# Kernel optimization log

Measured on AMD Instinct MI355X. Metric: run time of the kernel, lower is better.

## Reference

```python
import jax, jax.numpy as jnp
import numpy as np

BINS = 30
MMT = 0.75
LOSS_WEIGHT = 1.0
N = 16_777_216


def setup_inputs() -> dict:
    key = jax.random.key(0)
    k1, k2 = jax.random.split(key)
    pred = jax.random.normal(k1, (N,), dtype=jnp.float32)
    target = jax.random.randint(k2, (N,), 0, 2, dtype=jnp.int32)
    acc_sum = jnp.zeros((BINS,), dtype=jnp.float32)  # momentum state, zeros at first call
    return {"pred": pred, "acc_sum": acc_sum, "target": target}


def reference(pred, acc_sum, target):
    # prob = sigmoid(pred); expand to binary channels [N,2]
    prob = jax.nn.sigmoid(pred)
    t = target.astype(jnp.float32)
    x = jnp.stack([prob, 1.0 - prob], axis=1)  # [N,2]  (original reassigns pred := probs)
    y = jnp.stack([t, 1.0 - t], axis=1)        # [N,2]

    g = jnp.abs(x - y)                          # gradient-norm proxy, in [0,1]
    total = jnp.maximum(jnp.asarray(x.size, jnp.float32), 1.0)  # all label_weights == 1

    # bin assignment: loop 'g>=e[i] & g<=e[i+1]' with later-bin overwrite == floor(g*bins)
    # edges[-1] += 1e-6 means g==1 lands in last bin -> clip to BINS-1
    bin_idx = jnp.clip((g * BINS).astype(jnp.int32), 0, BINS - 1)  # [N,2]

    counts = jnp.zeros((BINS,), jnp.float32).at[bin_idx.ravel()].add(1.0)
    nonempty = counts > 0
    n = jnp.maximum(jnp.sum(nonempty.astype(jnp.float32)), 1.0)

    # momentum update of acc_sum only for populated bins
    new_acc = jnp.where(nonempty, MMT * acc_sum + (1.0 - MMT) * counts, acc_sum)
    w_bin = jnp.where(nonempty, total / jnp.maximum(new_acc, 1e-12), 0.0) / n  # [BINS]
    weights = w_bin[bin_idx]  # [N,2] scatter of per-bin weights

    # BCE-with-logits applied to x (the probabilities), matching the original
    bce = jnp.logaddexp(0.0, x) - x * y
    loss = jnp.sum(weights * bce) / total
    return loss * LOSS_WEIGHT
```

## Files before the change

kernel.cpp:

```cpp
#include <hip/hip_runtime.h>
#include <math.h>

#define BINS 30
#define FGRID 256
#define FBLOCK 1024
#define FITERS 16
#define FNCOPIES 256
#define GGRID 2048
#define GBLOCK 256
#define GNCOPIES 64
#define CPW 16
#define CSTRIDE 31
#define GSCALE 4096.0f
#define CNT_SHIFT 21
#define CNT_ONE (2u << CNT_SHIFT)
#define GMASK 0x1FFFFFu


__device__ __forceinline__ void ghmc_elem(float p, int t, unsigned int* s_hist,
                                          unsigned int copy_base)
{
    float q = __int_as_float(__float_as_int(p) ^ (t << 31));
    float e = __expf(-q);
    float g = __builtin_amdgcn_rcpf(1.0f + e);
    int b = min((int)(g * 30.0f), BINS - 1);
    unsigned int pkt = CNT_ONE | (unsigned int)(g * GSCALE);
    atomicAdd(&s_hist[copy_base + b], pkt);
}

__device__ __forceinline__ void ghmc_vec4(float4 p, int4 t, unsigned int* s_hist,
                                          unsigned int copy_base)
{
    ghmc_elem(p.x, t.x, s_hist, copy_base);
    ghmc_elem(p.y, t.y, s_hist, copy_base);
    ghmc_elem(p.z, t.z, s_hist, copy_base);
    ghmc_elem(p.w, t.w, s_hist, copy_base);
}

__global__ __launch_bounds__(FBLOCK) void ghmc_pass1_big(
    const float* __restrict__ pred, const int* __restrict__ target,
    unsigned int* __restrict__ cnt_part, float* __restrict__ gs_part)
{
    __shared__ unsigned int s_hist[FNCOPIES * CSTRIDE];
    const int tid = threadIdx.x;
    const unsigned int copy_base = (((tid >> 6) << 4) + (tid & (CPW - 1))) * CSTRIDE;

    for (int i = tid; i < FNCOPIES * CSTRIDE; i += FBLOCK) s_hist[i] = 0u;
    __syncthreads();

    const float4* p4 = reinterpret_cast<const float4*>(pred);
    const int4*   t4 = reinterpret_cast<const int4*>(target);
    const int stride = FGRID * FBLOCK;
    const int idx = blockIdx.x * FBLOCK + tid;

    float4 pA = p4[idx], pB;
    int4   tA = t4[idx], tB;
    #pragma unroll
    for (int k = 0; k < FITERS; k += 2) {
        if (k + 1 < FITERS) { pB = p4[idx + (k + 1) * stride];
                              tB = t4[idx + (k + 1) * stride]; }
        __builtin_amdgcn_sched_barrier(0);
        ghmc_vec4(pA, tA, s_hist, copy_base);
        if (k + 2 < FITERS) { pA = p4[idx + (k + 2) * stride];
                              tA = t4[idx + (k + 2) * stride]; }
        __builtin_amdgcn_sched_barrier(0);
        if (k + 1 < FITERS) ghmc_vec4(pB, tB, s_hist, copy_base);
    }

    __syncthreads();
    if (tid < BINS) {
        unsigned int cnt = 0;
        float gs = 0.0f;
        #pragma unroll 8
        for (int c = 0; c < FNCOPIES; ++c) {
            unsigned int v = s_hist[c * CSTRIDE + tid];
            cnt += v >> CNT_SHIFT;
            gs  += (float)(v & GMASK);
        }
        cnt_part[blockIdx.x * BINS + tid] = cnt;
        gs_part [blockIdx.x * BINS + tid] = gs * (1.0f / GSCALE);
    }
}

__global__ __launch_bounds__(1024) void ghmc_final_part(
    const unsigned int* __restrict__ cnt_part, const float* __restrict__ gs_part,
    const float* __restrict__ acc_sum, float* __restrict__ out, float total, int nwg)
{
    __shared__ unsigned int s_cnt[32];
    __shared__ float        s_gs[32];
    const int tid = threadIdx.x;
    const int bin = tid >> 5;
    const int j   = tid & 31;

    unsigned int c = 0;
    float        g = 0.0f;
    if (bin < BINS) {
        for (int w = j; w < nwg; w += 32) {
            c += cnt_part[w * BINS + bin];
            g += gs_part [w * BINS + bin];
        }
    }
    #pragma unroll
    for (int off = 16; off > 0; off >>= 1) {
        c += __shfl_xor(c, off);
        g += __shfl_xor(g, off);
    }
    if (bin < BINS && j == 0) { s_cnt[bin] = c; s_gs[bin] = g; }
    __syncthreads();

    if (tid < 64) {
        bool nonempty = (tid < BINS) && (s_cnt[tid] > 0u);
        float nb = fmaxf((float)__popcll(__ballot(nonempty)), 1.0f);

        float val = 0.0f;
        if (nonempty) {
            float cc    = (float)s_cnt[tid];
            float elems = 0.5f * cc;
            float gmean = s_gs[tid] / elems;
            float F = log1pf(expf(gmean)) + log1pf(expf(1.0f - gmean)) - 1.0f + gmean;
            float new_acc = 0.75f * acc_sum[tid] + 0.25f * cc;
            float w = (total / fmaxf(new_acc, 1e-12f)) / nb;
            val = w * elems * F;
        }
        #pragma unroll
        for (int off = 32; off > 0; off >>= 1) val += __shfl_down(val, off);
        if (tid == 0) out[0] = val / total;
    }
}

__global__ __launch_bounds__(GBLOCK) void ghmc_pass1_gen(
    const float* __restrict__ pred, const int* __restrict__ target,
    unsigned int* __restrict__ g_cnt, float* __restrict__ g_gsum,
    int n4, int n)
{
    __shared__ unsigned int s_hist[GNCOPIES * CSTRIDE];
    const int tid = threadIdx.x;
    const unsigned int copy_base = (((tid >> 6) << 4) + (tid & (CPW - 1))) * CSTRIDE;
    for (int i = tid; i < GNCOPIES * CSTRIDE; i += GBLOCK) s_hist[i] = 0u;
    __syncthreads();

    const int gid    = blockIdx.x * GBLOCK + tid;
    const int stride = gridDim.x * GBLOCK;
    for (int i = gid; i < n4; i += stride) {
        float4 p = reinterpret_cast<const float4*>(pred)[i];
        int4   t = reinterpret_cast<const int4*>(target)[i];
        ghmc_vec4(p, t, s_hist, copy_base);
    }
    if (blockIdx.x == 0) {
        for (int i = n4 * 4 + tid; i < n; i += GBLOCK)
            ghmc_elem(pred[i], target[i], s_hist, copy_base);
    }

    __syncthreads();
    if (tid < BINS) {
        unsigned int cnt = 0;
        float gs = 0.0f;
        #pragma unroll
        for (int c = 0; c < GNCOPIES; ++c) {
            unsigned int v = s_hist[c * CSTRIDE + tid];
            cnt += v >> CNT_SHIFT;
            gs  += (float)(v & GMASK);
        }
        atomicAdd(&g_cnt[tid], cnt);
        atomicAdd(&g_gsum[tid], gs * (1.0f / GSCALE));
    }
}

__global__ __launch_bounds__(64) void ghmc_final_atomic(
    const unsigned int* __restrict__ counts, const float* __restrict__ gsums,
    const float* __restrict__ acc_sum, float* __restrict__ out, float total)
{
    const int tid = threadIdx.x;
    bool nonempty = (tid < BINS) && (counts[tid] > 0u);
    float nb = fmaxf((float)__popcll(__ballot(nonempty)), 1.0f);

    float val = 0.0f;
    if (nonempty) {
        float cc    = (float)counts[tid];
        float elems = 0.5f * cc;
        float gmean = gsums[tid] / elems;
        float F = log1pf(expf(gmean)) + log1pf(expf(1.0f - gmean)) - 1.0f + gmean;
        float new_acc = 0.75f * acc_sum[tid] + 0.25f * cc;
        float w = (total / fmaxf(new_acc, 1e-12f)) / nb;
        val = w * elems * F;
    }
    #pragma unroll
    for (int off = 32; off > 0; off >>= 1) val += __shfl_down(val, off);
    if (tid == 0) out[0] = val / total;
}

extern "C" void kernel_launch(void* const* d_in, const int* in_sizes, int n_in,
                              void* d_out, int out_size, void* d_ws, size_t ws_size,
                              hipStream_t stream) {
    const float* pred    = (const float*)d_in[0];
    const float* acc_sum = (const float*)d_in[1];
    const int*   target  = (const int*)d_in[2];
    float* out = (float*)d_out;

    int n = in_sizes[0];
    float total = fmaxf(2.0f * (float)n, 1.0f);

    const size_t fast_ws = (size_t)FGRID * BINS * 8;
    if (n == FGRID * FBLOCK * FITERS * 4 && ws_size >= fast_ws) {
        unsigned int* cnt_part = (unsigned int*)d_ws;
        float*        gs_part  = (float*)((unsigned int*)d_ws + FGRID * BINS);
        ghmc_pass1_big<<<FGRID, FBLOCK, 0, stream>>>(pred, target, cnt_part, gs_part);
        ghmc_final_part<<<1, 1024, 0, stream>>>(cnt_part, gs_part, acc_sum, out, total, FGRID);
    } else {
        int n4 = n / 4;
        unsigned int* g_cnt  = (unsigned int*)d_ws;
        float*        g_gsum = (float*)d_ws + BINS;
        hipMemsetAsync(d_ws, 0, 2 * BINS * sizeof(float), stream);
        ghmc_pass1_gen<<<GGRID, GBLOCK, 0, stream>>>(pred, target, g_cnt, g_gsum, n4, n);
        ghmc_final_atomic<<<1, 64, 0, stream>>>(g_cnt, g_gsum, acc_sum, out, total);
    }
}
```

Measured before the change: 34.86 us.

## Deepen load pipeline with inline-asm loads and parallelize per-block histogram reduction

The main loop now issues raw global_load_dwordx4 instructions three iterations ahead into a 4-deep register ring, with explicit s_waitcnt vmcnt counts, replacing the previous two-stage software pipeline. The goal is more outstanding memory requests per thread, so HBM latency is better hidden in this bandwidth-bound pass. The end-of-block reduction over 256 histogram copies moves from 30 serial threads to 30 warps of 32 lanes, each summing 8 copies and then doing a shuffle reduction, with the grad sum kept as an integer. Hand-written asm with manual waitcnt is fragile: the compiler does not track these loads, and any vmcnt miscount can read registers before the data arrives.

```diff
diff --git a/kernel.cpp b/kernel.cpp
--- a/kernel.cpp
+++ b/kernel.cpp
@@ -6,6 +6,7 @@
 #define FBLOCK 1024
 #define FITERS 16
 #define FNCOPIES 256
+#define VSTEP (FGRID * FBLOCK * 16)
 #define GGRID 2048
 #define GBLOCK 256
 #define GNCOPIES 64
@@ -48,37 +49,55 @@
     for (int i = tid; i < FNCOPIES * CSTRIDE; i += FBLOCK) s_hist[i] = 0u;
     __syncthreads();
 
-    const float4* p4 = reinterpret_cast<const float4*>(pred);
-    const int4*   t4 = reinterpret_cast<const int4*>(target);
-    const int stride = FGRID * FBLOCK;
-    const int idx = blockIdx.x * FBLOCK + tid;
-
-    float4 pA = p4[idx], pB;
-    int4   tA = t4[idx], tB;
+    const unsigned int voff0 = (unsigned int)((blockIdx.x * FBLOCK + tid) * 16);
+
+    float4 pb[4];
+    int4   tb[4];
+
+#define ISSUE(k)                                                               \
+    do {                                                                       \
+        asm volatile("global_load_dwordx4 %0, %1, %2"                          \
+                     : "=v"(pb[(k) & 3])                                       \
+                     : "v"(voff0 + (unsigned)(k) * (unsigned)VSTEP), "s"(pred)); \
+        asm volatile("global_load_dwordx4 %0, %1, %2"                          \
+                     : "=v"(tb[(k) & 3])                                       \
+                     : "v"(voff0 + (unsigned)(k) * (unsigned)VSTEP), "s"(target)); \
+    } while (0)
+
+    ISSUE(0); ISSUE(1); ISSUE(2);
+
     #pragma unroll
-    for (int k = 0; k < FITERS; k += 2) {
-        if (k + 1 < FITERS) { pB = p4[idx + (k + 1) * stride];
-                              tB = t4[idx + (k + 1) * stride]; }
+    for (int k = 0; k < FITERS; ++k) {
+        if (k + 3 < FITERS) ISSUE(k + 3);
+        asm volatile("s_waitcnt vmcnt(%0)"
+                     :: "i"((k + 3 < FITERS) ? 6 : 2 * (FITERS - 1 - k)));
         __builtin_amdgcn_sched_barrier(0);
-        ghmc_vec4(pA, tA, s_hist, copy_base);
-        if (k + 2 < FITERS) { pA = p4[idx + (k + 2) * stride];
-                              tA = t4[idx + (k + 2) * stride]; }
-        __builtin_amdgcn_sched_barrier(0);
-        if (k + 1 < FITERS) ghmc_vec4(pB, tB, s_hist, copy_base);
-    }
-
-    __syncthreads();
-    if (tid < BINS) {
-        unsigned int cnt = 0;
-        float gs = 0.0f;
-        #pragma unroll 8
-        for (int c = 0; c < FNCOPIES; ++c) {
-            unsigned int v = s_hist[c * CSTRIDE + tid];
-            cnt += v >> CNT_SHIFT;
-            gs  += (float)(v & GMASK);
-        }
-        cnt_part[blockIdx.x * BINS + tid] = cnt;
-        gs_part [blockIdx.x * BINS + tid] = gs * (1.0f / GSCALE);
+        ghmc_vec4(pb[k & 3], tb[k & 3], s_hist, copy_base);
+    }
+#undef ISSUE
+
+    __syncthreads();
+    {
+        const int bin   = tid >> 5;
+        const int chunk = tid & 31;
+        if (bin < BINS) {
+            unsigned int c = 0, g = 0;
+            #pragma unroll
+            for (int j = 0; j < 8; ++j) {
+                unsigned int v = s_hist[(chunk * 8 + j) * CSTRIDE + bin];
+                c += v >> CNT_SHIFT;
+                g += v & GMASK;
+            }
+            #pragma unroll
+            for (int off = 16; off > 0; off >>= 1) {
+                c += __shfl_xor(c, off);
+                g += __shfl_xor(g, off);
+            }
+            if (chunk == 0) {
+                cnt_part[blockIdx.x * BINS + bin] = c;
+                gs_part [blockIdx.x * BINS + bin] = (float)g * (1.0f / GSCALE);
+            }
+        }
     }
 }
 
```

Measured after the change: 32.15 us. -7.8%, faster.
